# Performance work log

Measured on AMD Instinct MI355X. Metric: run time of the kernel, lower is better.

The kernel has to match this reference:

```python
import jax, jax.numpy as jnp
import numpy as np
from jax import lax

NUM_ENTITIES = 100000
NUM_RELATIONS = 500
EMBED_DIM = 512
NUM_FILTERS = 32
KERNEL_SIZE = 3
BATCH = 8192
CONV_OUT_DIM = NUM_FILTERS * (2 * EMBED_DIM - KERNEL_SIZE + 1)  # 32704


def setup_inputs() -> dict:
    key = jax.random.key(0)
    ks = jax.random.split(key, 8)
    entity_emb = jax.random.normal(ks[0], (NUM_ENTITIES, EMBED_DIM), dtype=jnp.float32) * 0.01
    rel_emb = jax.random.normal(ks[1], (NUM_RELATIONS, EMBED_DIM), dtype=jnp.float32) * 0.01
    conv_weight = jax.random.normal(ks[2], (NUM_FILTERS, KERNEL_SIZE, 1), dtype=jnp.float32) * 0.1
    conv_bias = jnp.zeros((NUM_FILTERS,), dtype=jnp.float32)
    fc = jax.random.normal(ks[3], (CONV_OUT_DIM, EMBED_DIM), dtype=jnp.float32) * 0.01
    fc_bias = jnp.zeros((EMBED_DIM,), dtype=jnp.float32)
    subj = jax.random.randint(ks[4], (BATCH,), 0, NUM_ENTITIES)
    rel = jax.random.randint(ks[5], (BATCH,), 0, NUM_RELATIONS)
    obj = jax.random.randint(ks[6], (BATCH,), 0, NUM_ENTITIES)
    triples = jnp.stack([subj, rel, obj], axis=1).astype(jnp.int64)
    return {
        "entity_emb": entity_emb,
        "rel_emb": rel_emb,
        "conv_weight": conv_weight,
        "conv_bias": conv_bias,
        "fc": fc,
        "fc_bias": fc_bias,
        "triples": triples,
    }


def reference(entity_emb, rel_emb, conv_weight, conv_bias, fc, fc_bias, triples):
    # Gather embeddings for subject / relation / object
    subj_e = entity_emb[triples[:, 0]]          # (B, D)
    rel_e = rel_emb[triples[:, 1]]              # (B, D)
    obj_e = entity_emb[triples[:, 2]]           # (B, D)

    combined = jnp.concatenate([subj_e, rel_e], axis=-1)  # (B, 2D)

    # 1D valid convolution, single input channel. Original loops over output
    # positions with per-patch einsums; this is the vectorized equivalent:
    # conv_out[b, f, i] = sum_k combined[b, i+k] * conv_weight[f, k, 0]
    lhs = combined[:, None, :]                  # (B, 1, 2D)  NCH
    rhs = conv_weight                            # (F, K, 1) -> (F, 1, K) OIH
    rhs = jnp.transpose(conv_weight, (0, 2, 1))
    conv_out = lax.conv_general_dilated(
        lhs, rhs, window_strides=(1,), padding="VALID",
        dimension_numbers=("NCH", "OIH", "NCH"))  # (B, F, 2D-K+1)

    conv_out = jax.nn.relu(conv_out + conv_bias[None, :, None])
    conv_flat = conv_out.reshape(conv_out.shape[0], -1)    # (B, F*(2D-K+1))

    projected = conv_flat @ fc + fc_bias                   # (B, D)
    scores = jnp.sum(projected * obj_e, axis=-1)           # (B,)
    return scores
```

## Files before the change

### kernel.cpp

```cpp
#include <hip/hip_runtime.h>
#include <hip/hip_bf16.h>


#define ND    512
#define NF    32
#define NP    1022
#define KTOT  32704
#define NB    8192
#define BM    128
#define BN    256
#define BK    64
#define NSTEPS 511

typedef __attribute__((ext_vector_type(8))) short bf16x8;
typedef __attribute__((ext_vector_type(4))) float f32x4;

typedef const __attribute__((address_space(1))) unsigned int* gas1_p;
typedef __attribute__((address_space(3))) unsigned int* las3_p;

__device__ __forceinline__ void gload_lds16(const void* g, const void* l) {
  __builtin_amdgcn_global_load_lds((gas1_p)(unsigned long long)(uintptr_t)g,
                                   (las3_p)(unsigned int)(uintptr_t)l, 16, 0, 0);
}

__device__ __forceinline__ unsigned int pack_bf16x2(float a, float b) {
  __hip_bfloat162 hh = __float22bfloat162_rn(make_float2(a, b));
  unsigned int u;
  __builtin_memcpy(&u, &hh, 4);
  return u;
}

__global__ __launch_bounds__(256) void k_gather(const float* __restrict__ ent,
                                                const float* __restrict__ rel,
                                                const int* __restrict__ trip,
                                                float* __restrict__ comb) {
  int b = blockIdx.x, t = threadIdx.x;
  int s = trip[b * 3 + 0], r = trip[b * 3 + 1];
  float4 v;
  if (t < 128) v = ((const float4*)(ent + (size_t)s * ND))[t];
  else         v = ((const float4*)(rel + (size_t)r * ND))[t - 128];
  ((float4*)(comb + (size_t)b * 1024))[t] = v;
}

__global__ __launch_bounds__(256) void k_fcT(const float* __restrict__ fc,
                                             unsigned short* __restrict__ fcT) {
  __shared__ float tile[32][132];
  int p = blockIdx.x >> 2, dt = blockIdx.x & 3;
  int d0 = dt * 128, t = threadIdx.x;
  int f = t >> 3, l8 = t & 7;
  const float* src = fc + ((size_t)f * NP + p) * ND + d0 + l8 * 16;
#pragma unroll
  for (int j = 0; j < 4; ++j) {
    float4 v = *(const float4*)(src + j * 4);
    *(float4*)&tile[f][l8 * 16 + j * 4] = v;
  }
  __syncthreads();
  if (t < 128) {
    unsigned int outw[16];
#pragma unroll
    for (int fq = 0; fq < 16; ++fq)
      outw[fq] = pack_bf16x2(tile[2 * fq][t], tile[2 * fq + 1][t]);
    unsigned short* dst = fcT + (size_t)(d0 + t) * KTOT + p * NF;
#pragma unroll
    for (int i = 0; i < 4; ++i) {
      uint4 w;
      w.x = outw[i * 4 + 0]; w.y = outw[i * 4 + 1];
      w.z = outw[i * 4 + 2]; w.w = outw[i * 4 + 3];
      *(uint4*)((char*)dst + i * 16) = w;
    }
  }
}

__global__ __launch_bounds__(512, 4) void k_gemm(
    const float* __restrict__ comb, const unsigned short* __restrict__ fcT,
    const float* __restrict__ cw, const float* __restrict__ cb,
    const float* __restrict__ fcb, const int* __restrict__ trip,
    const float* __restrict__ ent, float* __restrict__ out) {
  __shared__ unsigned short Al[BM * BK];
  __shared__ unsigned short Bl[BN * BK];
  __shared__ float wk[3 * 32];
  __shared__ float wb[32];

  const int tid = threadIdx.x;
  const int bid = blockIdx.x;
  const int xcd = bid & 7;
  const int n_blk = xcd >> 2, ksp = xcd & 3, m_blk = bid >> 3;

  if (tid < 96) wk[(tid % 3) * 32 + (tid / 3)] = cw[tid];
  if (tid < 32) wb[tid] = cb[tid];

  const int m_local = tid >> 2;
  const int sub = tid & 3;
  const int h = sub >> 1;
  const int fh = sub & 1;
  const float* crow = comb + (size_t)(m_blk * BM + m_local) * 1024;

  const int wv = tid >> 6, lane = tid & 63;
  const int wm = wv >> 2, wn = wv & 3;
  const int r16 = lane & 15, rq = lane >> 4;

  f32x4 acc[4][4];
#pragma unroll
  for (int i = 0; i < 4; ++i)
#pragma unroll
    for (int j = 0; j < 4; ++j)
      acc[i][j] = (f32x4)0.0f;

  const int s_begin = (NSTEPS * ksp) >> 2;
  const int s_end   = (NSTEPS * (ksp + 1)) >> 2;

  __syncthreads();

  float2 c01 = *(const float2*)(crow + 2 * s_begin);
  float2 c23 = *(const float2*)(crow + 2 * s_begin + 2);

  for (int s = s_begin; s < s_end; ++s) {
    const int k0 = s * BK;

#pragma unroll
    for (int r = 0; r < 4; ++r) {
      int c = r * 512 + tid;
      int dl = c >> 3, kq = c & 7;
      int kqs = kq ^ (dl & 7);
      const unsigned short* src =
          fcT + (size_t)(n_blk * BN + dl) * KTOT + (k0 + kqs * 8);
      gload_lds16(src, Bl + (size_t)(r * 512 + wv * 64) * 8);
    }

    float ca, cbv, ccv;
    if (h == 0) { ca = c01.x; cbv = c01.y; ccv = c23.x; }
    else        { ca = c01.y; cbv = c23.x; ccv = c23.y; }
    unsigned int pk[8];
#pragma unroll
    for (int j = 0; j < 8; ++j) {
      int f0 = fh * 16 + 2 * j, f1 = f0 + 1;
      float v0 = fmaxf(0.f, wb[f0] + wk[f0] * ca + wk[32 + f0] * cbv + wk[64 + f0] * ccv);
      float v1 = fmaxf(0.f, wb[f1] + wk[f1] * ca + wk[32 + f1] * cbv + wk[64 + f1] * ccv);
      pk[j] = pack_bf16x2(v0, v1);
    }
#pragma unroll
    for (int i = 0; i < 2; ++i) {
      int slot = (h * 4 + fh * 2 + i) ^ (m_local & 7);
      uint4 w;
      w.x = pk[i * 4 + 0]; w.y = pk[i * 4 + 1];
      w.z = pk[i * 4 + 2]; w.w = pk[i * 4 + 3];
      *(uint4*)((char*)Al + m_local * 128 + slot * 16) = w;
    }

    if (s + 1 < s_end) {
      c01 = *(const float2*)(crow + 2 * (s + 1));
      c23 = *(const float2*)(crow + 2 * (s + 1) + 2);
    }

    __syncthreads();

    bf16x8 af[4][2], bfr[4][2];
#pragma unroll
    for (int mi = 0; mi < 4; ++mi) {
      int row = wm * 64 + mi * 16 + r16;
#pragma unroll
      for (int ks = 0; ks < 2; ++ks) {
        int slot = (ks * 4 + rq) ^ (row & 7);
        af[mi][ks] = *(const bf16x8*)((const char*)Al + row * 128 + slot * 16);
      }
    }
#pragma unroll
    for (int ni = 0; ni < 4; ++ni) {
      int dl = wn * 64 + ni * 16 + r16;
#pragma unroll
      for (int ks = 0; ks < 2; ++ks) {
        int slot = (ks * 4 + rq) ^ (dl & 7);
        bfr[ni][ks] = *(const bf16x8*)((const char*)Bl + dl * 128 + slot * 16);
      }
    }
#pragma unroll
    for (int ks = 0; ks < 2; ++ks)
#pragma unroll
      for (int mi = 0; mi < 4; ++mi)
#pragma unroll
        for (int ni = 0; ni < 4; ++ni)
          acc[mi][ni] = __builtin_amdgcn_mfma_f32_16x16x32_bf16(
              af[mi][ks], bfr[ni][ks], acc[mi][ni], 0, 0, 0);

    __syncthreads();
  }

  const int colbase = n_blk * BN + wn * 64;
#pragma unroll
  for (int mi = 0; mi < 4; ++mi) {
#pragma unroll
    for (int rr = 0; rr < 4; ++rr) {
      int row = m_blk * BM + wm * 64 + mi * 16 + rq * 4 + rr;
      int oid = trip[row * 3 + 2];
      const float* orow = ent + (size_t)oid * ND + colbase;
      float part = 0.f;
#pragma unroll
      for (int ni = 0; ni < 4; ++ni) {
        int d = ni * 16 + r16;
        float v = acc[mi][ni][rr];
        if (ksp == 0) v += fcb[colbase + d];
        part += v * orow[d];
      }
      part += __shfl_xor(part, 1);
      part += __shfl_xor(part, 2);
      part += __shfl_xor(part, 4);
      part += __shfl_xor(part, 8);
      if (r16 == 0) atomicAdd(out + row, part);
    }
  }
}

extern "C" void kernel_launch(void* const* d_in, const int* in_sizes, int n_in,
                              void* d_out, int out_size, void* d_ws, size_t ws_size,
                              hipStream_t stream) {
  const float* ent = (const float*)d_in[0];
  const float* rel = (const float*)d_in[1];
  const float* cw  = (const float*)d_in[2];
  const float* cb  = (const float*)d_in[3];
  const float* fc  = (const float*)d_in[4];
  const float* fcb = (const float*)d_in[5];
  const int*   trp = (const int*)d_in[6];
  float* out = (float*)d_out;

  float* comb = (float*)d_ws;
  unsigned short* fcT = (unsigned short*)((char*)d_ws + (size_t)NB * 1024 * 4);

  hipMemsetAsync(d_out, 0, (size_t)out_size * sizeof(float), stream);
  k_gather<<<NB, 256, 0, stream>>>(ent, rel, trp, comb);
  k_fcT<<<NP * 4, 256, 0, stream>>>(fc, fcT);
  k_gemm<<<512, 512, 0, stream>>>(comb, fcT, cw, cb, fcb, trp, ent, out);
}
```

Baseline: 612.3 us.

## Double-buffer B tile and software-pipeline A generation in GEMM loop

Double-buffers the fcT tile in LDS so the next K-step's global-to-LDS loads are issued before the current step's MFMAs. The on-the-fly conv+ReLU A-tile generation for the next step moves after the MFMAs, with comb values prefetched two steps ahead. The thread mapping for A generation changes so each wave holds its conv weights and biases in registers instead of reading them from LDS, and MFMA issue gets raised wave priority. The cost is double the B LDS footprint, which may reduce occupancy, plus more registers, and the loop still has two barriers per step.

```diff
diff --git a/kernel.cpp b/kernel.cpp
--- a/kernel.cpp
+++ b/kernel.cpp
@@ -28,6 +28,24 @@
   unsigned int u;
   __builtin_memcpy(&u, &hh, 4);
   return u;
+}
+
+__device__ __forceinline__ uint4 gen8(float tA, float tB, float tC,
+    const float4& W0, const float4& W1, const float4& W2,
+    const float4& W3, const float4& W4, const float4& W5,
+    const float4& Bb0, const float4& Bb1) {
+  float v0 = fmaxf(0.f, Bb0.x + W0.x * tA + W0.y * tB + W0.z * tC);
+  float v1 = fmaxf(0.f, Bb0.y + W0.w * tA + W1.x * tB + W1.y * tC);
+  float v2 = fmaxf(0.f, Bb0.z + W1.z * tA + W1.w * tB + W2.x * tC);
+  float v3 = fmaxf(0.f, Bb0.w + W2.y * tA + W2.z * tB + W2.w * tC);
+  float v4 = fmaxf(0.f, Bb1.x + W3.x * tA + W3.y * tB + W3.z * tC);
+  float v5 = fmaxf(0.f, Bb1.y + W3.w * tA + W4.x * tB + W4.y * tC);
+  float v6 = fmaxf(0.f, Bb1.z + W4.z * tA + W4.w * tB + W5.x * tC);
+  float v7 = fmaxf(0.f, Bb1.w + W5.y * tA + W5.z * tB + W5.w * tC);
+  uint4 w;
+  w.x = pack_bf16x2(v0, v1); w.y = pack_bf16x2(v2, v3);
+  w.z = pack_bf16x2(v4, v5); w.w = pack_bf16x2(v6, v7);
+  return w;
 }
 
 __global__ __launch_bounds__(256) void k_gather(const float* __restrict__ ent,
@@ -76,29 +94,30 @@
     const float* __restrict__ cw, const float* __restrict__ cb,
     const float* __restrict__ fcb, const int* __restrict__ trip,
     const float* __restrict__ ent, float* __restrict__ out) {
+  __shared__ unsigned short Bl[2][BN * BK];
   __shared__ unsigned short Al[BM * BK];
-  __shared__ unsigned short Bl[BN * BK];
-  __shared__ float wk[3 * 32];
-  __shared__ float wb[32];
 
   const int tid = threadIdx.x;
   const int bid = blockIdx.x;
   const int xcd = bid & 7;
   const int n_blk = xcd >> 2, ksp = xcd & 3, m_blk = bid >> 3;
 
-  if (tid < 96) wk[(tid % 3) * 32 + (tid / 3)] = cw[tid];
-  if (tid < 32) wb[tid] = cb[tid];
-
-  const int m_local = tid >> 2;
-  const int sub = tid & 3;
-  const int h = sub >> 1;
-  const int fh = sub & 1;
-  const float* crow = comb + (size_t)(m_blk * BM + m_local) * 1024;
-
   const int wv = tid >> 6, lane = tid & 63;
   const int wm = wv >> 2, wn = wv & 3;
   const int r16 = lane & 15, rq = lane >> 4;
 
+  const int q = wv & 3, h = wv >> 2;
+  const int qu = __builtin_amdgcn_readfirstlane(q);
+  const float4* wp = (const float4*)(cw + qu * 24);
+  const float4 W0 = wp[0], W1 = wp[1], W2 = wp[2], W3 = wp[3], W4 = wp[4], W5 = wp[5];
+  const float4* bp = (const float4*)(cb + qu * 8);
+  const float4 Bb0 = bp[0], Bb1 = bp[1];
+  const int word = h * 4 + q;
+
+  const int r0 = lane, r1 = lane + 64;
+  const float* crow0 = comb + (size_t)(m_blk * BM + r0) * 1024;
+  const float* crow1 = comb + (size_t)(m_blk * BM + r1) * 1024;
+
   f32x4 acc[4][4];
 #pragma unroll
   for (int i = 0; i < 4; ++i)
@@ -106,54 +125,64 @@
     for (int j = 0; j < 4; ++j)
       acc[i][j] = (f32x4)0.0f;
 
-  const int s_begin = (NSTEPS * ksp) >> 2;
-  const int s_end   = (NSTEPS * (ksp + 1)) >> 2;
-
-  __syncthreads();
-
-  float2 c01 = *(const float2*)(crow + 2 * s_begin);
-  float2 c23 = *(const float2*)(crow + 2 * s_begin + 2);
-
-  for (int s = s_begin; s < s_end; ++s) {
-    const int k0 = s * BK;
-
+  const int sb = (NSTEPS * ksp) >> 2;
+  const int se = (NSTEPS * (ksp + 1)) >> 2;
+
+  float2 p01a = *(const float2*)(crow0 + 2 * sb);
+  float2 p23a = *(const float2*)(crow0 + 2 * sb + 2);
+  float2 p45a = *(const float2*)(crow0 + 2 * sb + 4);
+  float2 p01b = *(const float2*)(crow1 + 2 * sb);
+  float2 p23b = *(const float2*)(crow1 + 2 * sb + 2);
+  float2 p45b = *(const float2*)(crow1 + 2 * sb + 4);
+
+  {
+    const int k0 = sb * BK;
 #pragma unroll
     for (int r = 0; r < 4; ++r) {
       int c = r * 512 + tid;
-      int dl = c >> 3, kq = c & 7;
-      int kqs = kq ^ (dl & 7);
+      int dl = c >> 3, kq = c & 7, kqs = kq ^ (dl & 7);
       const unsigned short* src =
           fcT + (size_t)(n_blk * BN + dl) * KTOT + (k0 + kqs * 8);
-      gload_lds16(src, Bl + (size_t)(r * 512 + wv * 64) * 8);
-    }
-
-    float ca, cbv, ccv;
-    if (h == 0) { ca = c01.x; cbv = c01.y; ccv = c23.x; }
-    else        { ca = c01.y; cbv = c23.x; ccv = c23.y; }
-    unsigned int pk[8];
-#pragma unroll
-    for (int j = 0; j < 8; ++j) {
-      int f0 = fh * 16 + 2 * j, f1 = f0 + 1;
-      float v0 = fmaxf(0.f, wb[f0] + wk[f0] * ca + wk[32 + f0] * cbv + wk[64 + f0] * ccv);
-      float v1 = fmaxf(0.f, wb[f1] + wk[f1] * ca + wk[32 + f1] * cbv + wk[64 + f1] * ccv);
-      pk[j] = pack_bf16x2(v0, v1);
-    }
-#pragma unroll
-    for (int i = 0; i < 2; ++i) {
-      int slot = (h * 4 + fh * 2 + i) ^ (m_local & 7);
-      uint4 w;
-      w.x = pk[i * 4 + 0]; w.y = pk[i * 4 + 1];
-      w.z = pk[i * 4 + 2]; w.w = pk[i * 4 + 3];
-      *(uint4*)((char*)Al + m_local * 128 + slot * 16) = w;
-    }
-
-    if (s + 1 < s_end) {
-      c01 = *(const float2*)(crow + 2 * (s + 1));
-      c23 = *(const float2*)(crow + 2 * (s + 1) + 2);
-    }
-
-    __syncthreads();
-
+      gload_lds16(src, &Bl[sb & 1][0] + (size_t)(r * 512 + wv * 64) * 8);
+    }
+  }
+  {
+    float tA0 = h ? p01a.y : p01a.x, tB0 = h ? p23a.x : p01a.y, tC0 = h ? p23a.y : p23a.x;
+    float tA1 = h ? p01b.y : p01b.x, tB1 = h ? p23b.x : p01b.y, tC1 = h ? p23b.y : p23b.x;
+    uint4 wA = gen8(tA0, tB0, tC0, W0, W1, W2, W3, W4, W5, Bb0, Bb1);
+    uint4 wB = gen8(tA1, tB1, tC1, W0, W1, W2, W3, W4, W5, Bb0, Bb1);
+    *(uint4*)((char*)Al + r0 * 128 + ((word ^ (r0 & 7)) * 16)) = wA;
+    *(uint4*)((char*)Al + r1 * 128 + ((word ^ (r1 & 7)) * 16)) = wB;
+  }
+  float ac0 = p23a.x, ac1 = p23a.y, ac2 = p45a.x, ac3 = p45a.y;
+  float bc0 = p23b.x, bc1 = p23b.y, bc2 = p45b.x, bc3 = p45b.y;
+
+  __syncthreads();
+
+  for (int s = sb; s < se; ++s) {
+    const int cur = s & 1, nxt = cur ^ 1;
+    const bool more = (s + 1 < se);
+
+    float2 ea, eb;
+    if (s + 2 < se) {
+      ea = *(const float2*)(crow0 + 2 * s + 6);
+      eb = *(const float2*)(crow1 + 2 * s + 6);
+    }
+    __builtin_amdgcn_sched_barrier(0);
+
+    if (more) {
+      const int k0 = (s + 1) * BK;
+#pragma unroll
+      for (int r = 0; r < 4; ++r) {
+        int c = r * 512 + tid;
+        int dl = c >> 3, kq = c & 7, kqs = kq ^ (dl & 7);
+        const unsigned short* src =
+            fcT + (size_t)(n_blk * BN + dl) * KTOT + (k0 + kqs * 8);
+        gload_lds16(src, &Bl[nxt][0] + (size_t)(r * 512 + wv * 64) * 8);
+      }
+    }
+
+    const char* BlC = (const char*)&Bl[cur][0];
     bf16x8 af[4][2], bfr[4][2];
 #pragma unroll
     for (int mi = 0; mi < 4; ++mi) {
@@ -170,9 +199,10 @@
 #pragma unroll
       for (int ks = 0; ks < 2; ++ks) {
         int slot = (ks * 4 + rq) ^ (dl & 7);
-        bfr[ni][ks] = *(const bf16x8*)((const char*)Bl + dl * 128 + slot * 16);
-      }
-    }
+        bfr[ni][ks] = *(const bf16x8*)(BlC + dl * 128 + slot * 16);
+      }
+    }
+    __builtin_amdgcn_s_setprio(1);
 #pragma unroll
     for (int ks = 0; ks < 2; ++ks)
 #pragma unroll
@@ -181,8 +211,27 @@
         for (int ni = 0; ni < 4; ++ni)
           acc[mi][ni] = __builtin_amdgcn_mfma_f32_16x16x32_bf16(
               af[mi][ks], bfr[ni][ks], acc[mi][ni], 0, 0, 0);
-
-    __syncthreads();
+    __builtin_amdgcn_s_setprio(0);
+
+    __builtin_amdgcn_sched_barrier(0);
+    __builtin_amdgcn_s_barrier();
+
+    if (more) {
+      float tA0 = h ? ac1 : ac0, tB0 = h ? ac2 : ac1, tC0 = h ? ac3 : ac2;
+      float tA1 = h ? bc1 : bc0, tB1 = h ? bc2 : bc1, tC1 = h ? bc3 : bc2;
+      uint4 wA = gen8(tA0, tB0, tC0, W0, W1, W2, W3, W4, W5, Bb0, Bb1);
+      uint4 wB = gen8(tA1, tB1, tC1, W0, W1, W2, W3, W4, W5, Bb0, Bb1);
+      *(uint4*)((char*)Al + r0 * 128 + ((word ^ (r0 & 7)) * 16)) = wA;
+      *(uint4*)((char*)Al + r1 * 128 + ((word ^ (r1 & 7)) * 16)) = wB;
+      if (s + 2 < se) {
+        ac0 = ac2; ac1 = ac3; ac2 = ea.x; ac3 = ea.y;
+        bc0 = bc2; bc1 = bc3; bc2 = eb.x; bc3 = eb.y;
+      }
+    }
+
+    asm volatile("s_waitcnt vmcnt(0) lgkmcnt(0)" ::: "memory");
+    __builtin_amdgcn_sched_barrier(0);
+    __builtin_amdgcn_s_barrier();
   }
 
   const int colbase = n_blk * BN + wn * 64;
```

After: 1.436 ms. 134% more time.
